# Performance work log

Hardware: AMD Instinct MI355X
Metric: run time of the kernel (lower is better)

Reference implementation:

```python
import jax, jax.numpy as jnp
import numpy as np
import math

N_HEADS = 8
INPUT_DIM = 128
EMBED_DIM = 128
KEY_DIM = EMBED_DIM // N_HEADS  # 16, val_dim == key_dim
BATCH = 4
GRAPH = 2048


def setup_inputs() -> dict:
    key = jax.random.key(0)
    k1, k2, k3, k4, k5 = jax.random.split(key, 5)
    h = jax.random.normal(k1, (BATCH, GRAPH, INPUT_DIM), dtype=jnp.float32)
    # torch.rand -> uniform [0,1)
    W_query = jax.random.uniform(k2, (N_HEADS, INPUT_DIM, KEY_DIM), dtype=jnp.float32)
    W_key = jax.random.uniform(k3, (N_HEADS, INPUT_DIM, KEY_DIM), dtype=jnp.float32)
    W_val = jax.random.uniform(k4, (N_HEADS, INPUT_DIM, KEY_DIM), dtype=jnp.float32)
    W_out = jax.random.uniform(k5, (N_HEADS, KEY_DIM, EMBED_DIM), dtype=jnp.float32)
    return {"h": h, "W_query": W_query, "W_key": W_key, "W_val": W_val, "W_out": W_out}


def reference(h, W_query, W_key, W_val, W_out):
    # q defaults to h (self-attention)
    norm = 1.0 / math.sqrt(KEY_DIM)
    # per-head projections: [H, B, N, dk]
    Q = jnp.einsum('bnd,hdk->hbnk', h, W_query)
    K = jnp.einsum('bnd,hdk->hbnk', h, W_key)
    V = jnp.einsum('bnd,hdv->hbnv', h, W_val)
    compat = norm * jnp.einsum('hbqk,hbnk->hbqn', Q, K)  # [H, B, Nq, N]
    attn = jax.nn.softmax(compat, axis=-1)
    heads = jnp.einsum('hbqn,hbnv->hbqv', attn, V)  # [H, B, Nq, dv]
    out = jnp.einsum('hbqv,hve->bqe', heads, W_out)  # [B, Nq, E]
    return out
```

## Files before the change

kernel.cpp:

```cpp
#include <hip/hip_runtime.h>

typedef __attribute__((ext_vector_type(4))) float f32x4;
typedef __attribute__((ext_vector_type(8))) short bf16x8;

constexpr int NH = 8, D = 128, DK = 16, B = 4, N = 2048;
constexpr int KTILE = 128;
constexpr int NTILES = N / KTILE;
constexpr int TILE_SHORTS = 6144;
constexpr float QSCALE = 0.36067376022224085f;

__device__ __forceinline__ unsigned short f2bf(float f) {
    union { float f; unsigned u; } v; v.f = f;
    return (unsigned short)((v.u + 0x7fffu + ((v.u >> 16) & 1u)) >> 16);
}
__device__ __forceinline__ float bf2f(unsigned short h) {
    union { unsigned u; float f; } v; v.u = ((unsigned)h) << 16; return v.f;
}
__device__ __forceinline__ unsigned pack2(float a, float b) {
    union { float f; unsigned u; } x, y; x.f = a; y.f = b;
    return (x.u >> 16) | (y.u & 0xFFFF0000u);
}
__device__ __forceinline__ float fexp2(float x) {
    float r; asm("v_exp_f32 %0, %1" : "=v"(r) : "v"(x)); return r;
}

__global__ __launch_bounds__(256) void wprep_kernel(
    const float* __restrict__ Wq, const float* __restrict__ Wk,
    const float* __restrict__ Wv, const float* __restrict__ Wo,
    unsigned short* __restrict__ Wf, unsigned short* __restrict__ Wof)
{
    const int t = blockIdx.x * 256 + threadIdx.x;
    if (t < 49152) {
        const int p = t >> 14, r = t & 16383;
        const int head = r >> 11, d = (r >> 4) & 127, kk = r & 15;
        const float wv = (p == 0 ? Wq : p == 1 ? Wk : Wv)[r];
        const unsigned short hi = f2bf(wv);
        const unsigned short lo = f2bf(wv - bf2f(hi));
        const int c = p * 8 + head, s = d >> 4, dd = d & 15;
        const int ch = dd >> 3, j = dd & 7;
        Wf[((c * 8 + s) * 64 + kk + 16 * ch) * 8 + j] = hi;
        Wf[((c * 8 + s) * 64 + kk + 16 * (2 + ch)) * 8 + j] = lo;
    } else {
        const int r = t - 49152;
        const int head = r >> 11, v = (r >> 7) & 15, e = r & 127;
        const float wv = Wo[r];
        const unsigned short hi = f2bf(wv);
        const unsigned short lo = f2bf(wv - bf2f(hi));
        const int c = e >> 4, s = head, ch = v >> 3, j = v & 7;
        Wof[((c * 8 + s) * 64 + (e & 15) + 16 * ch) * 8 + j] = hi;
        Wof[((c * 8 + s) * 64 + (e & 15) + 16 * (2 + ch)) * 8 + j] = lo;
    }
}

constexpr int GR = 32;
__global__ __launch_bounds__(256) void qkv_gemm(
    const float* __restrict__ h, const unsigned short* __restrict__ Wf,
    float* __restrict__ Q, unsigned short* __restrict__ KV)
{
    const int cg = blockIdx.x % 3;
    const int row0 = (blockIdx.x / 3) * GR;
    const int b = row0 >> 11, n0 = row0 & (N - 1);
    const int t = threadIdx.x, w = t >> 6, l = t & 63;
    __shared__ unsigned short hf[8][2][64][8];

    #pragma unroll
    for (int pass = 0; pass < 4; ++pass) {
        const int rb = pass * 8 + (t >> 5);
        const int d0 = (t & 31) * 4;
        float4 hv = *(const float4*)&h[(size_t)(row0 + rb) * D + d0];
        #pragma unroll
        for (int i = 0; i < 4; ++i) {
            const int d = d0 + i;
            const float x = ((const float*)&hv)[i];
            const unsigned short hi = f2bf(x);
            const unsigned short lo = f2bf(x - bf2f(hi));
            const int s = d >> 4, dd = d & 15, ch = dd >> 3, j = dd & 7;
            hf[s][rb >> 4][(rb & 15) + 16 * ch][j] = hi;
            hf[s][rb >> 4][(rb & 15) + 16 * (2 + ch)][j] = lo;
        }
    }
    __syncthreads();

    f32x4 acc[4];
    #pragma unroll
    for (int i = 0; i < 4; ++i) acc[i] = (f32x4){0.f, 0.f, 0.f, 0.f};

    for (int s = 0; s < 8; ++s) {
        bf16x8 b1 = *(const bf16x8*)&hf[s][w & 1][l][0];
        bf16x8 b2 = *(const bf16x8*)&hf[s][w & 1][l ^ 32][0];
        #pragma unroll
        for (int ct = 0; ct < 4; ++ct) {
            const int c = cg * 8 + (w >> 1) * 4 + ct;
            bf16x8 af = *(const bf16x8*)&Wf[((c * 8 + s) * 64 + l) * 8];
            acc[ct] = __builtin_amdgcn_mfma_f32_16x16x32_bf16(af, b1, acc[ct], 0, 0, 0);
            acc[ct] = __builtin_amdgcn_mfma_f32_16x16x32_bf16(af, b2, acc[ct], 0, 0, 0);
        }
    }

    const int n = n0 + (w & 1) * 16 + (l & 15);
    const int rl = n & 127;
    const int kk0 = (l >> 4) * 4;
    #pragma unroll
    for (int ct = 0; ct < 4; ++ct) {
        const int head = (w >> 1) * 4 + ct;
        const int hb = head * B + b;
        if (cg == 0) {
            float4 o;
            o.x = acc[ct][0]; o.y = acc[ct][1]; o.z = acc[ct][2]; o.w = acc[ct][3];
            *(float4*)&Q[((size_t)hb * N + n) * DK + kk0] = o;
        } else {
            unsigned short* tb = KV + (size_t)hb * NTILES * TILE_SHORTS
                               + (size_t)(n >> 7) * TILE_SHORTS;
            if (cg == 1) {
                const int gs = kk0 >> 3, j0 = kk0 & 7;
                const int kb2 = rl >> 5, kap = rl & 31;
                const int sub = 2 * kb2 + ((kap >> 2) & 1);
                const int row16 = 4 * (kap >> 3) + (kap & 3);
                ushort4 sh, sl;
                unsigned short* shp = (unsigned short*)&sh;
                unsigned short* slp = (unsigned short*)&sl;
                #pragma unroll
                for (int r = 0; r < 4; ++r) {
                    const unsigned short hi = f2bf(acc[ct][r]);
                    shp[r] = hi;
                    slp[r] = f2bf(acc[ct][r] - bf2f(hi));
                }
                *(ushort4*)&tb[sub * 512 + (row16 + 16 * gs) * 8 + j0] = sh;
                *(ushort4*)&tb[sub * 512 + (row16 + 16 * (2 + gs)) * 8 + j0] = sl;
            } else {
                #pragma unroll
                for (int r = 0; r < 4; ++r) {
                    const int kk = kk0 + r;
                    tb[4096 + kk * 128 + ((rl >> 3) ^ (kk & 7)) * 8 + (rl & 7)]
                        = f2bf(acc[ct][r]);
                }
            }
        }
    }
}

__global__ __launch_bounds__(256, 4) void attn_kernel(
    const float* __restrict__ Q, const unsigned short* __restrict__ KV,
    float* __restrict__ Hd)
{
    const int bid = blockIdx.x;
    const int hb = (bid & 7) * 4 + ((bid >> 3) >> 5);
    const int qt = (bid >> 3) & 31;
    const int t = threadIdx.x, w = t >> 6, l = t & 63;
    const int q16 = l & 15, g = l >> 4;
    const size_t qbase = (size_t)hb * N * DK;
    const char* kvb = (const char*)(KV + (size_t)hb * NTILES * TILE_SHORTS);

    __shared__ unsigned short smem[2][TILE_SHORTS];

    const int qrow = qt * 64 + w * 16 + q16;
    bf16x8 qhi, qlo;
    {
        const float* qp = Q + qbase + (size_t)qrow * DK + (g & 1) * 8;
        float4 qa = *(const float4*)qp, qb = *(const float4*)(qp + 4);
        #pragma unroll
        for (int i = 0; i < 8; ++i) {
            const float x = (i < 4 ? ((const float*)&qa)[i] : ((const float*)&qb)[i - 4]) * QSCALE;
            const unsigned short hi = f2bf(x);
            qhi[i] = (short)hi;
            qlo[i] = (short)f2bf(x - bf2f(hi));
        }
    }
    const bf16x8 qf1 = (g < 2) ? qhi : qlo;
    const bf16x8 qf2 = (g < 2) ? qlo : qhi;

    union { unsigned u[4]; bf16x8 v; } ones;
    #pragma unroll
    for (int i = 0; i < 4; ++i) ones.u[i] = 0x3F803F80u;

    f32x4 oacc = {0.f, 0.f, 0.f, 0.f};
    f32x4 lacc = {0.f, 0.f, 0.f, 0.f};
    float m = -3.0e38f;

    uint4 s0 = *(const uint4*)(kvb + t * 16);
    uint4 s1 = *(const uint4*)(kvb + 4096 + t * 16);
    uint4 s2 = *(const uint4*)(kvb + 8192 + t * 16);
    *(uint4*)((char*)&smem[0][0] + t * 16) = s0;
    *(uint4*)((char*)&smem[0][0] + 4096 + t * 16) = s1;
    *(uint4*)((char*)&smem[0][0] + 8192 + t * 16) = s2;

    int cur = 0;
    for (int tile = 0; tile < NTILES; ++tile) {
        __syncthreads();
        if (tile + 1 < NTILES) {
            const char* gt = kvb + (size_t)(tile + 1) * 12288;
            s0 = *(const uint4*)(gt + t * 16);
            s1 = *(const uint4*)(gt + 4096 + t * 16);
            s2 = *(const uint4*)(gt + 8192 + t * 16);
        }
        const char* buf = (const char*)&smem[cur][0];

        f32x4 aA[4], aB[4];
        const f32x4 z = {0.f, 0.f, 0.f, 0.f};
        __builtin_amdgcn_s_setprio(1);
        #pragma unroll
        for (int kb = 0; kb < 4; ++kb) {
            bf16x8 kA = *(const bf16x8*)(buf + (2 * kb) * 1024 + l * 16);
            bf16x8 kB = *(const bf16x8*)(buf + (2 * kb + 1) * 1024 + l * 16);
            aA[kb] = __builtin_amdgcn_mfma_f32_16x16x32_bf16(kA, qf1, z, 0, 0, 0);
            aA[kb] = __builtin_amdgcn_mfma_f32_16x16x32_bf16(kA, qf2, aA[kb], 0, 0, 0);
            aB[kb] = __builtin_amdgcn_mfma_f32_16x16x32_bf16(kB, qf1, z, 0, 0, 0);
            aB[kb] = __builtin_amdgcn_mfma_f32_16x16x32_bf16(kB, qf2, aB[kb], 0, 0, 0);
        }
        __builtin_amdgcn_s_setprio(0);

        float tm = -3.0e38f;
        #pragma unroll
        for (int kb = 0; kb < 4; ++kb) {
            tm = fmaxf(tm, fmaxf(fmaxf(aA[kb][0], aA[kb][1]), fmaxf(aA[kb][2], aA[kb][3])));
            tm = fmaxf(tm, fmaxf(fmaxf(aB[kb][0], aB[kb][1]), fmaxf(aB[kb][2], aB[kb][3])));
        }
        tm = fmaxf(tm, __shfl_xor(tm, 16));
        tm = fmaxf(tm, __shfl_xor(tm, 32));
        if (!__all(tm - m <= 8.0f)) {
            const float nm = fmaxf(m, tm);
            const float sc = fexp2(m - nm);
            m = nm;
            oacc *= sc;
            lacc *= sc;
        }
        #pragma unroll
        for (int kb = 0; kb < 4; ++kb) {
            #pragma unroll
            for (int i = 0; i < 4; ++i) {
                aA[kb][i] = fexp2(aA[kb][i] - m);
                aB[kb][i] = fexp2(aB[kb][i] - m);
            }
        }
        __builtin_amdgcn_s_setprio(1);
        #pragma unroll
        for (int kb = 0; kb < 4; ++kb) {
            union { unsigned u[4]; bf16x8 v; } pf;
            pf.u[0] = pack2(aA[kb][0], aA[kb][1]);
            pf.u[1] = pack2(aA[kb][2], aA[kb][3]);
            pf.u[2] = pack2(aB[kb][0], aB[kb][1]);
            pf.u[3] = pack2(aB[kb][2], aB[kb][3]);
            bf16x8 vf = *(const bf16x8*)(buf + 8192 + q16 * 256 + (((kb * 4 + g) ^ (q16 & 7)) * 16));
            oacc = __builtin_amdgcn_mfma_f32_16x16x32_bf16(vf, pf.v, oacc, 0, 0, 0);
            lacc = __builtin_amdgcn_mfma_f32_16x16x32_bf16(ones.v, pf.v, lacc, 0, 0, 0);
        }
        __builtin_amdgcn_s_setprio(0);

        if (tile + 1 < NTILES) {
            char* nb = (char*)&smem[cur ^ 1][0];
            *(uint4*)(nb + t * 16) = s0;
            *(uint4*)(nb + 4096 + t * 16) = s1;
            *(uint4*)(nb + 8192 + t * 16) = s2;
        }
        cur ^= 1;
    }

    const float invl = 1.f / lacc[0];
    float4 o;
    o.x = oacc[0] * invl; o.y = oacc[1] * invl;
    o.z = oacc[2] * invl; o.w = oacc[3] * invl;
    *(float4*)(Hd + qbase + (size_t)qrow * DK + g * 4) = o;
}

constexpr int OGR = 16;
__global__ __launch_bounds__(256) void out_gemm(
    const float* __restrict__ Hd, const unsigned short* __restrict__ Wof,
    float* __restrict__ out)
{
    const int row0 = blockIdx.x * OGR;
    const int b = row0 >> 11, n0 = row0 & (N - 1);
    const int t = threadIdx.x, w = t >> 6, l = t & 63;
    __shared__ unsigned short hf[8][64][8];

    #pragma unroll
    for (int pass = 0; pass < 2; ++pass) {
        const int rb = pass * 8 + (t >> 5);
        const int d0 = (t & 31) * 4;
        float4 hv = *(const float4*)&Hd[((size_t)((d0 >> 4) * B + b) * N + (n0 + rb)) * DK + (d0 & 15)];
        #pragma unroll
        for (int i = 0; i < 4; ++i) {
            const int d = d0 + i;
            const float x = ((const float*)&hv)[i];
            const unsigned short hi = f2bf(x);
            const unsigned short lo = f2bf(x - bf2f(hi));
            const int s = d >> 4, dd = d & 15, ch = dd >> 3, j = dd & 7;
            hf[s][rb + 16 * ch][j] = hi;
            hf[s][rb + 16 * (2 + ch)][j] = lo;
        }
    }
    __syncthreads();

    f32x4 acc[2];
    #pragma unroll
    for (int i = 0; i < 2; ++i) acc[i] = (f32x4){0.f, 0.f, 0.f, 0.f};

    for (int s = 0; s < 8; ++s) {
        bf16x8 b1 = *(const bf16x8*)&hf[s][l][0];
        bf16x8 b2 = *(const bf16x8*)&hf[s][l ^ 32][0];
        #pragma unroll
        for (int ct = 0; ct < 2; ++ct) {
            const int c = w * 2 + ct;
            bf16x8 af = *(const bf16x8*)&Wof[((c * 8 + s) * 64 + l) * 8];
            acc[ct] = __builtin_amdgcn_mfma_f32_16x16x32_bf16(af, b1, acc[ct], 0, 0, 0);
            acc[ct] = __builtin_amdgcn_mfma_f32_16x16x32_bf16(af, b2, acc[ct], 0, 0, 0);
        }
    }

    const int n = row0 + (l & 15);
    #pragma unroll
    for (int ct = 0; ct < 2; ++ct) {
        const int c = w * 2 + ct;
        float4 o;
        o.x = acc[ct][0]; o.y = acc[ct][1]; o.z = acc[ct][2]; o.w = acc[ct][3];
        *(float4*)&out[(size_t)n * D + c * 16 + (l >> 4) * 4] = o;
    }
}

extern "C" void kernel_launch(void* const* d_in, const int* in_sizes, int n_in,
                              void* d_out, int out_size, void* d_ws, size_t ws_size,
                              hipStream_t stream) {
    const float* h  = (const float*)d_in[0];
    const float* Wq = (const float*)d_in[1];
    const float* Wk = (const float*)d_in[2];
    const float* Wv = (const float*)d_in[3];
    const float* Wo = (const float*)d_in[4];
    float* out = (float*)d_out;

    char* ws = (char*)d_ws;
    float* Q = (float*)ws;
    unsigned short* KV  = (unsigned short*)(ws + (size_t)4 * 1024 * 1024);
    unsigned short* Wf  = (unsigned short*)(ws + (size_t)10 * 1024 * 1024);
    unsigned short* Wof = (unsigned short*)(ws + (size_t)10 * 1024 * 1024 + 196608);

    wprep_kernel<<<256, 256, 0, stream>>>(Wq, Wk, Wv, Wo, Wf, Wof);
    qkv_gemm<<<(B * N / GR) * 3, 256, 0, stream>>>(h, Wf, Q, KV);
    attn_kernel<<<NH * B * 32, 256, 0, stream>>>(Q, KV, Q);
    out_gemm<<<B * N / OGR, 256, 0, stream>>>(Q, Wof, out);
}
```

Before: 60.85 us.

## Software-pipeline attention: overlap previous tile's PV MFMAs with current QK

Restructures the attention loop so the P·V and row-sum MFMAs for the previous tile are issued right after the Q·K MFMAs of the current tile. The packed probabilities are carried across iterations in registers, and a final PV step is added after the loop. LDS grows to three K/V buffers, with global prefetch running two tiles ahead and a single barrier per iteration. It also replaces the max reduction with v_max3_f32 inline asm. The cost is more LDS per block and about 16 extra VGPRs, which could pressure occupancy under the 4-blocks-per-CU launch bound.

```diff
diff --git a/kernel.cpp b/kernel.cpp
--- a/kernel.cpp
+++ b/kernel.cpp
@@ -22,6 +22,10 @@
 }
 __device__ __forceinline__ float fexp2(float x) {
     float r; asm("v_exp_f32 %0, %1" : "=v"(r) : "v"(x)); return r;
+}
+__device__ __forceinline__ float fmax3(float a, float b, float c) {
+    float r; asm("v_max3_f32 %0, %1, %2, %3" : "=v"(r) : "v"(a), "v"(b), "v"(c));
+    return r;
 }
 
 __global__ __launch_bounds__(256) void wprep_kernel(
@@ -151,7 +155,7 @@
     const size_t qbase = (size_t)hb * N * DK;
     const char* kvb = (const char*)(KV + (size_t)hb * NTILES * TILE_SHORTS);
 
-    __shared__ unsigned short smem[2][TILE_SHORTS];
+    __shared__ unsigned short smem[3][TILE_SHORTS];
 
     const int qrow = qt * 64 + w * 16 + q16;
     bf16x8 qhi, qlo;
@@ -176,45 +180,75 @@
     f32x4 oacc = {0.f, 0.f, 0.f, 0.f};
     f32x4 lacc = {0.f, 0.f, 0.f, 0.f};
     float m = -3.0e38f;
-
-    uint4 s0 = *(const uint4*)(kvb + t * 16);
-    uint4 s1 = *(const uint4*)(kvb + 4096 + t * 16);
-    uint4 s2 = *(const uint4*)(kvb + 8192 + t * 16);
-    *(uint4*)((char*)&smem[0][0] + t * 16) = s0;
-    *(uint4*)((char*)&smem[0][0] + 4096 + t * 16) = s1;
-    *(uint4*)((char*)&smem[0][0] + 8192 + t * 16) = s2;
-
-    int cur = 0;
+    unsigned pf_prev[16];
+
+    char* b_cur = (char*)&smem[0][0];
+    char* b_nxt = (char*)&smem[1][0];
+    char* b_prv = (char*)&smem[2][0];
+
+    uint4 s0, s1, s2;
+    {
+        const char* gt = kvb;
+        s0 = *(const uint4*)(gt + t * 16);
+        s1 = *(const uint4*)(gt + 4096 + t * 16);
+        s2 = *(const uint4*)(gt + 8192 + t * 16);
+        *(uint4*)(b_cur + t * 16) = s0;
+        *(uint4*)(b_cur + 4096 + t * 16) = s1;
+        *(uint4*)(b_cur + 8192 + t * 16) = s2;
+        const char* g1 = kvb + 12288;
+        s0 = *(const uint4*)(g1 + t * 16);
+        s1 = *(const uint4*)(g1 + 4096 + t * 16);
+        s2 = *(const uint4*)(g1 + 8192 + t * 16);
+    }
+    __syncthreads();
+
     for (int tile = 0; tile < NTILES; ++tile) {
-        __syncthreads();
-        if (tile + 1 < NTILES) {
-            const char* gt = kvb + (size_t)(tile + 1) * 12288;
-            s0 = *(const uint4*)(gt + t * 16);
-            s1 = *(const uint4*)(gt + 4096 + t * 16);
-            s2 = *(const uint4*)(gt + 8192 + t * 16);
-        }
-        const char* buf = (const char*)&smem[cur][0];
-
         f32x4 aA[4], aB[4];
         const f32x4 z = {0.f, 0.f, 0.f, 0.f};
         __builtin_amdgcn_s_setprio(1);
         #pragma unroll
         for (int kb = 0; kb < 4; ++kb) {
-            bf16x8 kA = *(const bf16x8*)(buf + (2 * kb) * 1024 + l * 16);
-            bf16x8 kB = *(const bf16x8*)(buf + (2 * kb + 1) * 1024 + l * 16);
+            bf16x8 kA = *(const bf16x8*)(b_cur + (2 * kb) * 1024 + l * 16);
+            bf16x8 kB = *(const bf16x8*)(b_cur + (2 * kb + 1) * 1024 + l * 16);
             aA[kb] = __builtin_amdgcn_mfma_f32_16x16x32_bf16(kA, qf1, z, 0, 0, 0);
             aA[kb] = __builtin_amdgcn_mfma_f32_16x16x32_bf16(kA, qf2, aA[kb], 0, 0, 0);
             aB[kb] = __builtin_amdgcn_mfma_f32_16x16x32_bf16(kB, qf1, z, 0, 0, 0);
             aB[kb] = __builtin_amdgcn_mfma_f32_16x16x32_bf16(kB, qf2, aB[kb], 0, 0, 0);
         }
+        if (tile > 0) {
+            #pragma unroll
+            for (int kb = 0; kb < 4; ++kb) {
+                union { unsigned u[4]; bf16x8 v; } pf;
+                pf.u[0] = pf_prev[4 * kb + 0]; pf.u[1] = pf_prev[4 * kb + 1];
+                pf.u[2] = pf_prev[4 * kb + 2]; pf.u[3] = pf_prev[4 * kb + 3];
+                bf16x8 vf = *(const bf16x8*)(b_prv + 8192 + q16 * 256 + (((kb * 4 + g) ^ (q16 & 7)) * 16));
+                oacc = __builtin_amdgcn_mfma_f32_16x16x32_bf16(vf, pf.v, oacc, 0, 0, 0);
+                lacc = __builtin_amdgcn_mfma_f32_16x16x32_bf16(ones.v, pf.v, lacc, 0, 0, 0);
+            }
+        }
         __builtin_amdgcn_s_setprio(0);
 
-        float tm = -3.0e38f;
-        #pragma unroll
-        for (int kb = 0; kb < 4; ++kb) {
-            tm = fmaxf(tm, fmaxf(fmaxf(aA[kb][0], aA[kb][1]), fmaxf(aA[kb][2], aA[kb][3])));
-            tm = fmaxf(tm, fmaxf(fmaxf(aB[kb][0], aB[kb][1]), fmaxf(aB[kb][2], aB[kb][3])));
-        }
+        if (tile + 1 < NTILES) {
+            *(uint4*)(b_nxt + t * 16) = s0;
+            *(uint4*)(b_nxt + 4096 + t * 16) = s1;
+            *(uint4*)(b_nxt + 8192 + t * 16) = s2;
+        }
+        if (tile + 2 < NTILES) {
+            const char* gt = kvb + (size_t)(tile + 2) * 12288;
+            s0 = *(const uint4*)(gt + t * 16);
+            s1 = *(const uint4*)(gt + 4096 + t * 16);
+            s2 = *(const uint4*)(gt + 8192 + t * 16);
+        }
+
+        float t0 = fmax3(fmax3(aA[0][0], aA[0][1], aA[0][2]),
+                         fmax3(aA[0][3], aB[0][0], aB[0][1]), fmaxf(aB[0][2], aB[0][3]));
+        float t1 = fmax3(fmax3(aA[1][0], aA[1][1], aA[1][2]),
+                         fmax3(aA[1][3], aB[1][0], aB[1][1]), fmaxf(aB[1][2], aB[1][3]));
+        float t2 = fmax3(fmax3(aA[2][0], aA[2][1], aA[2][2]),
+                         fmax3(aA[2][3], aB[2][0], aB[2][1]), fmaxf(aB[2][2], aB[2][3]));
+        float t3 = fmax3(fmax3(aA[3][0], aA[3][1], aA[3][2]),
+                         fmax3(aA[3][3], aB[3][0], aB[3][1]), fmaxf(aB[3][2], aB[3][3]));
+        float tm = fmaxf(fmax3(t0, t1, t2), t3);
         tm = fmaxf(tm, __shfl_xor(tm, 16));
         tm = fmaxf(tm, __shfl_xor(tm, 32));
         if (!__all(tm - m <= 8.0f)) {
@@ -232,27 +266,26 @@
                 aB[kb][i] = fexp2(aB[kb][i] - m);
             }
         }
-        __builtin_amdgcn_s_setprio(1);
         #pragma unroll
         for (int kb = 0; kb < 4; ++kb) {
-            union { unsigned u[4]; bf16x8 v; } pf;
-            pf.u[0] = pack2(aA[kb][0], aA[kb][1]);
-            pf.u[1] = pack2(aA[kb][2], aA[kb][3]);
-            pf.u[2] = pack2(aB[kb][0], aB[kb][1]);
-            pf.u[3] = pack2(aB[kb][2], aB[kb][3]);
-            bf16x8 vf = *(const bf16x8*)(buf + 8192 + q16 * 256 + (((kb * 4 + g) ^ (q16 & 7)) * 16));
-            oacc = __builtin_amdgcn_mfma_f32_16x16x32_bf16(vf, pf.v, oacc, 0, 0, 0);
-            lacc = __builtin_amdgcn_mfma_f32_16x16x32_bf16(ones.v, pf.v, lacc, 0, 0, 0);
-        }
-        __builtin_amdgcn_s_setprio(0);
-
-        if (tile + 1 < NTILES) {
-            char* nb = (char*)&smem[cur ^ 1][0];
-            *(uint4*)(nb + t * 16) = s0;
-            *(uint4*)(nb + 4096 + t * 16) = s1;
-            *(uint4*)(nb + 8192 + t * 16) = s2;
-        }
-        cur ^= 1;
+            pf_prev[4 * kb + 0] = pack2(aA[kb][0], aA[kb][1]);
+            pf_prev[4 * kb + 1] = pack2(aA[kb][2], aA[kb][3]);
+            pf_prev[4 * kb + 2] = pack2(aB[kb][0], aB[kb][1]);
+            pf_prev[4 * kb + 3] = pack2(aB[kb][2], aB[kb][3]);
+        }
+
+        __syncthreads();
+        char* tmp = b_prv; b_prv = b_cur; b_cur = b_nxt; b_nxt = tmp;
+    }
+
+    #pragma unroll
+    for (int kb = 0; kb < 4; ++kb) {
+        union { unsigned u[4]; bf16x8 v; } pf;
+        pf.u[0] = pf_prev[4 * kb + 0]; pf.u[1] = pf_prev[4 * kb + 1];
+        pf.u[2] = pf_prev[4 * kb + 2]; pf.u[3] = pf_prev[4 * kb + 3];
+        bf16x8 vf = *(const bf16x8*)(b_prv + 8192 + q16 * 256 + (((kb * 4 + g) ^ (q16 & 7)) * 16));
+        oacc = __builtin_amdgcn_mfma_f32_16x16x32_bf16(vf, pf.v, oacc, 0, 0, 0);
+        lacc = __builtin_amdgcn_mfma_f32_16x16x32_bf16(ones.v, pf.v, lacc, 0, 0, 0);
     }
 
     const float invl = 1.f / lacc[0];
```

Measured after the change: 61.12 us. Within noise of the previous version (+0.5%).

## Split attention KV range across two blocks and merge partials in output GEMM

Applied to the files above, without the earlier changes.

Each attention block now processes half of the key/value tiles for its query tile, doubling the grid. It writes unnormalized outputs plus per-row max and sum to workspace. The output GEMM merges the two partials with log-sum-exp rescaling before projection. This aims to raise parallelism and shorten per-block serial loops, at the cost of extra global traffic for partials and merge arithmetic.

```diff
diff --git a/kernel.cpp b/kernel.cpp
--- a/kernel.cpp
+++ b/kernel.cpp
@@ -6,6 +6,8 @@
 constexpr int NH = 8, D = 128, DK = 16, B = 4, N = 2048;
 constexpr int KTILE = 128;
 constexpr int NTILES = N / KTILE;
+constexpr int NSPLIT = 2;
+constexpr int TPS = NTILES / NSPLIT;
 constexpr int TILE_SHORTS = 6144;
 constexpr float QSCALE = 0.36067376022224085f;
 
@@ -22,6 +24,10 @@
 }
 __device__ __forceinline__ float fexp2(float x) {
     float r; asm("v_exp_f32 %0, %1" : "=v"(r) : "v"(x)); return r;
+}
+__device__ __forceinline__ float fmax3(float a, float b, float c) {
+    float r; asm("v_max3_f32 %0, %1, %2, %3" : "=v"(r) : "v"(a), "v"(b), "v"(c));
+    return r;
 }
 
 __global__ __launch_bounds__(256) void wprep_kernel(
@@ -141,15 +147,18 @@
 
 __global__ __launch_bounds__(256, 4) void attn_kernel(
     const float* __restrict__ Q, const unsigned short* __restrict__ KV,
-    float* __restrict__ Hd)
+    float* __restrict__ Opart, float2* __restrict__ ML)
 {
     const int bid = blockIdx.x;
-    const int hb = (bid & 7) * 4 + ((bid >> 3) >> 5);
-    const int qt = (bid >> 3) & 31;
+    const int inner = bid >> 3;
+    const int hb = (bid & 7) * 4 + (inner >> 6);
+    const int qt = (inner >> 1) & 31;
+    const int sp = inner & 1;
     const int t = threadIdx.x, w = t >> 6, l = t & 63;
     const int q16 = l & 15, g = l >> 4;
     const size_t qbase = (size_t)hb * N * DK;
-    const char* kvb = (const char*)(KV + (size_t)hb * NTILES * TILE_SHORTS);
+    const char* kvb = (const char*)(KV + (size_t)hb * NTILES * TILE_SHORTS)
+                    + (size_t)sp * TPS * 12288;
 
     __shared__ unsigned short smem[2][TILE_SHORTS];
 
@@ -185,9 +194,9 @@
     *(uint4*)((char*)&smem[0][0] + 8192 + t * 16) = s2;
 
     int cur = 0;
-    for (int tile = 0; tile < NTILES; ++tile) {
+    for (int tile = 0; tile < TPS; ++tile) {
         __syncthreads();
-        if (tile + 1 < NTILES) {
+        if (tile + 1 < TPS) {
             const char* gt = kvb + (size_t)(tile + 1) * 12288;
             s0 = *(const uint4*)(gt + t * 16);
             s1 = *(const uint4*)(gt + 4096 + t * 16);
@@ -246,7 +255,7 @@
         }
         __builtin_amdgcn_s_setprio(0);
 
-        if (tile + 1 < NTILES) {
+        if (tile + 1 < TPS) {
             char* nb = (char*)&smem[cur ^ 1][0];
             *(uint4*)(nb + t * 16) = s0;
             *(uint4*)(nb + 4096 + t * 16) = s1;
@@ -255,32 +264,43 @@
         cur ^= 1;
     }
 
-    const float invl = 1.f / lacc[0];
+    const size_t ro = ((size_t)sp * 32 + hb) * N + qrow;
     float4 o;
-    o.x = oacc[0] * invl; o.y = oacc[1] * invl;
-    o.z = oacc[2] * invl; o.w = oacc[3] * invl;
-    *(float4*)(Hd + qbase + (size_t)qrow * DK + g * 4) = o;
+    o.x = oacc[0]; o.y = oacc[1]; o.z = oacc[2]; o.w = oacc[3];
+    *(float4*)&Opart[ro * DK + g * 4] = o;
+    if (l < 16)
+        ML[ro] = make_float2(m, lacc[0]);
 }
 
 constexpr int OGR = 16;
 __global__ __launch_bounds__(256) void out_gemm(
-    const float* __restrict__ Hd, const unsigned short* __restrict__ Wof,
-    float* __restrict__ out)
+    const float* __restrict__ Opart, const float2* __restrict__ ML,
+    const unsigned short* __restrict__ Wof, float* __restrict__ out)
 {
     const int row0 = blockIdx.x * OGR;
     const int b = row0 >> 11, n0 = row0 & (N - 1);
     const int t = threadIdx.x, w = t >> 6, l = t & 63;
     __shared__ unsigned short hf[8][64][8];
+    constexpr size_t SPLITO = (size_t)32 * N * DK;
 
     #pragma unroll
     for (int pass = 0; pass < 2; ++pass) {
         const int rb = pass * 8 + (t >> 5);
         const int d0 = (t & 31) * 4;
-        float4 hv = *(const float4*)&Hd[((size_t)((d0 >> 4) * B + b) * N + (n0 + rb)) * DK + (d0 & 15)];
+        const int head = d0 >> 4, hb = head * B + b;
+        const size_t base = ((size_t)hb * N + (n0 + rb)) * DK + (d0 & 15);
+        float4 o0 = *(const float4*)&Opart[base];
+        float4 o1 = *(const float4*)&Opart[SPLITO + base];
+        const float2 ml0 = ML[(size_t)hb * N + (n0 + rb)];
+        const float2 ml1 = ML[(size_t)32 * N + (size_t)hb * N + (n0 + rb)];
+        const float M = fmaxf(ml0.x, ml1.x);
+        const float w0 = fexp2(ml0.x - M), w1 = fexp2(ml1.x - M);
+        const float inv = 1.f / (ml0.y * w0 + ml1.y * w1);
+        const float a0 = w0 * inv, a1 = w1 * inv;
         #pragma unroll
         for (int i = 0; i < 4; ++i) {
+            const float x = ((const float*)&o0)[i] * a0 + ((const float*)&o1)[i] * a1;
             const int d = d0 + i;
-            const float x = ((const float*)&hv)[i];
             const unsigned short hi = f2bf(x);
             const unsigned short lo = f2bf(x - bf2f(hi));
             const int s = d >> 4, dd = d & 15, ch = dd >> 3, j = dd & 7;
@@ -331,9 +351,11 @@
     unsigned short* KV  = (unsigned short*)(ws + (size_t)4 * 1024 * 1024);
     unsigned short* Wf  = (unsigned short*)(ws + (size_t)10 * 1024 * 1024);
     unsigned short* Wof = (unsigned short*)(ws + (size_t)10 * 1024 * 1024 + 196608);
+    float* Opart = (float*)(ws + (size_t)11 * 1024 * 1024);
+    float2* ML   = (float2*)(ws + (size_t)19 * 1024 * 1024);
 
     wprep_kernel<<<256, 256, 0, stream>>>(Wq, Wk, Wv, Wo, Wf, Wof);
     qkv_gemm<<<(B * N / GR) * 3, 256, 0, stream>>>(h, Wf, Q, KV);
-    attn_kernel<<<NH * B * 32, 256, 0, stream>>>(Q, KV, Q);
-    out_gemm<<<B * N / OGR, 256, 0, stream>>>(Q, Wof, out);
-}
+    attn_kernel<<<NH * B * 32 * NSPLIT, 256, 0, stream>>>(Q, KV, Opart, ML);
+    out_gemm<<<B * N / OGR, 256, 0, stream>>>(Opart, ML, Wof, out);
+}
```

Result: no change. 61.59 us (+1.2%).
